# Optimization experiments

Hardware: AMD Instinct MI355X
Metric: run time of the kernel (lower is better)

## Reference

```python
import jax, jax.numpy as jnp
import numpy as np

B, L, D_MODEL, D_FF, H = 2, 2048, 512, 512, 8
DK = D_FF // H


def _lin(key, fan_in, fan_out):
    k1, k2 = jax.random.split(key)
    lim = 1.0 / np.sqrt(fan_in)
    W = jax.random.uniform(k1, (fan_in, fan_out), jnp.float32, -lim, lim)
    b = jax.random.uniform(k2, (fan_out,), jnp.float32, -lim, lim)
    return W, b


def setup_inputs() -> dict:
    key = jax.random.key(0)
    ks = jax.random.split(key, 13)
    x = jax.random.normal(ks[0], (B, L, D_MODEL), jnp.float32)
    x_knowledge = jax.random.normal(ks[1], (B, L, D_MODEL), jnp.float32)
    Wv, bv = _lin(ks[2], D_MODEL, D_FF)
    Wk, bk = _lin(ks[3], D_MODEL, D_FF)
    Wq, bq = _lin(ks[4], D_MODEL, D_FF)
    Wkf, bkf = _lin(ks[5], D_MODEL, D_FF)
    Wqf, bqf = _lin(ks[6], D_MODEL, D_FF)
    Wq2, bq2 = _lin(ks[7], D_FF, D_FF)
    Wk2, bk2 = _lin(ks[8], D_FF, D_FF)
    Wkf2, bkf2 = _lin(ks[9], D_FF, D_FF)
    Wqf2, bqf2 = _lin(ks[10], D_FF, D_FF)
    Wo, bo = _lin(ks[11], D_FF, D_MODEL)
    return dict(x=x, x_knowledge=x_knowledge, Wv=Wv, bv=bv, Wk=Wk, bk=bk,
                Wq=Wq, bq=bq, Wkf=Wkf, bkf=bkf, Wqf=Wqf, bqf=bqf,
                Wq2=Wq2, bq2=bq2, Wk2=Wk2, bk2=bk2, Wqf2=Wqf2, bqf2=bqf2,
                Wkf2=Wkf2, bkf2=bkf2, Wo=Wo, bo=bo)


def reference(x, x_knowledge, Wv, bv, Wk, bk, Wq, bq, Wkf, bkf, Wqf, bqf,
              Wq2, bq2, Wk2, bk2, Wqf2, bqf2, Wkf2, bkf2, Wo, bo):
    b, l, _ = x.shape
    # first projections from d_model -> d_ff
    v = x @ Wv + bv
    k = x @ Wk + bk
    q = x @ Wq + bq
    k_fei = x_knowledge @ Wkf + bkf
    q_fei = x_knowledge @ Wqf + bqf
    # second projections + NONSTANDARD head split: raw reshape (B,L,d_ff)->(B,h,L,dk)
    q = (q @ Wq2 + bq2).reshape(b, H, l, DK)
    k = (k @ Wk2 + bk2).reshape(b, H, l, DK)
    q_fei = (q_fei @ Wqf2 + bqf2).reshape(b, H, l, DK)
    k_fei = (k_fei @ Wkf2 + bkf2).reshape(b, H, l, DK)
    scale = 1.0 / np.sqrt(2.0 * DK).astype(np.float32)
    att = jnp.einsum('bhld,bhmd->bhlm', q, k) * scale
    att_fei = jnp.einsum('bhld,bhmd->bhlm', q_fei, k_fei) * scale
    score = jax.nn.softmax(att + att_fei, axis=-1)  # dropout is identity at eval
    v = v.reshape(b, H, l, DK)
    out = jnp.einsum('bhlm,bhmd->bhld', score, v).reshape(b, l, D_FF)
    return out @ Wo + bo
```

## Files before the change

kernel.cpp:

```cpp
#include <hip/hip_runtime.h>
#include <hip/hip_bf16.h>

typedef unsigned short u16;
typedef unsigned int   u32;
typedef __attribute__((ext_vector_type(8))) short bf16x8;
typedef __attribute__((ext_vector_type(4))) float f32x4;

#define SCALE 0.08838834764831845f
#define SCLOG 0.12752040542575836f

__device__ inline u16 f2bf(float f) {
  u32 u = __builtin_bit_cast(u32, f);
  u = (u + 0x7FFFu + ((u >> 16) & 1u)) >> 16;
  return (u16)u;
}
__device__ inline float bf2f(u16 b) {
  u32 u = (u32)b << 16;
  return __builtin_bit_cast(float, u);
}
__device__ inline u32 pkbf(float a, float b) {
  return (u32)f2bf(a) | ((u32)f2bf(b) << 16);
}

__device__ __forceinline__ void glds16(const u16* g, u16* l) {
  __builtin_amdgcn_global_load_lds(
      (__attribute__((address_space(1))) void*)g,
      (__attribute__((address_space(3))) void*)l, 16, 0, 0);
}

__global__ __launch_bounds__(256) void cvt_bf16(const float* __restrict__ a,
                                                const float* __restrict__ b,
                                                u16* __restrict__ oa,
                                                u16* __restrict__ ob) {
  const float* in = blockIdx.y ? b : a;
  u16* out = blockIdx.y ? ob : oa;
  const int i = (blockIdx.x * 256 + threadIdx.x) * 8;
  float4 f0 = *(const float4*)(in + i);
  float4 f1 = *(const float4*)(in + i + 4);
  alignas(16) u16 t[8] = {f2bf(f0.x), f2bf(f0.y), f2bf(f0.z), f2bf(f0.w),
                          f2bf(f1.x), f2bf(f1.y), f2bf(f1.z), f2bf(f1.w)};
  *(uint4*)(out + i) = *(const uint4*)t;
}

struct TPtrs { const float* p[10]; };

__global__ __launch_bounds__(256) void transposeW(TPtrs ptrs, u16* __restrict__ out) {
  __shared__ u16 ts[64][65];
  const float sc = (blockIdx.z == 5 || blockIdx.z == 7) ? SCLOG : 1.0f;
  const float* in = ptrs.p[blockIdx.z];
  u16* o = out + (size_t)blockIdx.z * 262144;
  const int t = threadIdx.x;
  const int k0 = blockIdx.y * 64, n0 = blockIdx.x * 64;
  for (int pp = 0; pp < 16; ++pp) {
    int id = t + 256 * pp; int r = id >> 6, c = id & 63;
    ts[r][c] = f2bf(in[(size_t)(k0 + r) * 512 + n0 + c] * sc);
  }
  __syncthreads();
  for (int pp = 0; pp < 16; ++pp) {
    int id = t + 256 * pp; int r = id >> 6, c = id & 63;
    o[(size_t)(n0 + r) * 512 + k0 + c] = ts[c][r];
  }
}

struct BPtrs { const float* p[10]; };

__global__ __launch_bounds__(512) void biasPack(BPtrs bp, float* __restrict__ out) {
  const int z = blockIdx.x, n = threadIdx.x;
  const float sc = (z == 5 || z == 7) ? SCLOG : 1.0f;
  out[z * 512 + n] = bp.p[z][n] * sc;
}

__global__ __launch_bounds__(256) void transposeV(const u16* __restrict__ v1,
                                                  u16* __restrict__ vt) {
  __shared__ u16 ts[64][65];
  const size_t base = (size_t)blockIdx.y * 131072;
  const u16* in = v1 + base;
  u16* out = vt + base;
  const int l0 = blockIdx.x * 64;
  const int t = threadIdx.x;
  const int r = t >> 3, c8 = (t & 7) * 8;
  for (int pp = 0; pp < 2; ++pp) {
    int rr = r + pp * 32;
    *(uint4*)&ts[rr][c8] = *(const uint4*)&in[(size_t)(l0 + rr) * 64 + c8];
  }
  __syncthreads();
  for (int pp = 0; pp < 2; ++pp) {
    int d = r + pp * 32;
    alignas(16) u16 tmp[8];
    #pragma unroll
    for (int i = 0; i < 8; ++i) tmp[i] = ts[c8 + i][d];
    *(uint4*)&out[(size_t)d * 2048 + l0 + c8] = *(const uint4*)tmp;
  }
}

struct GemmBatch {
  const u16* A[4];
  const u16* Ax;
  int xsplit;
  void* out[5];
  int wrow0, zstride;
};

template <typename TOUT>
__global__ __launch_bounds__(256, 4) void gemm4(GemmBatch gb,
    const u16* __restrict__ Wt, const float* __restrict__ biasP) {
  const int tx = blockIdx.x, z = blockIdx.z;
  const u16* A = (tx < gb.xsplit) ? gb.A[z] : gb.Ax;
  const int wrow = gb.wrow0 + z * gb.zstride + tx * 128;
  const int m0 = blockIdx.y * 128;
  const u16* B = Wt + (size_t)wrow * 512;
  const float* bias = biasP + wrow;

  const int t = threadIdx.x, wid = t >> 6, lane = t & 63;
  const int lg = lane >> 4, ln = lane & 15;
  const int wr = wid >> 1, wc = wid & 1;

  __shared__ u16 As[128][64];
  __shared__ u16 Bs[128][64];

  const u16* Ag = A + (size_t)m0 * 512;
  const int lrow = lane >> 3, lch = lane & 7;

  f32x4 acc[4][4];
  #pragma unroll
  for (int i = 0; i < 4; ++i)
    #pragma unroll
    for (int j = 0; j < 4; ++j)
      #pragma unroll
      for (int r = 0; r < 4; ++r) acc[i][j][r] = 0.0f;

  for (int kt = 0; kt < 8; ++kt) {
    #pragma unroll
    for (int c = 0; c < 4; ++c) {
      const int row = (wid * 4 + c) * 8 + lrow;
      const size_t go = (size_t)row * 512 + kt * 64 + lch * 8;
      glds16(Ag + go, &As[(wid * 4 + c) * 8][0]);
      glds16(B  + go, &Bs[(wid * 4 + c) * 8][0]);
    }
    __syncthreads();

    #pragma unroll
    for (int ck = 0; ck < 2; ++ck) {
      bf16x8 af[4], bfr[4];
      #pragma unroll
      for (int mi = 0; mi < 4; ++mi)
        af[mi] = *(const bf16x8*)&As[wr * 64 + mi * 16 + ln][ck * 32 + lg * 8];
      #pragma unroll
      for (int ni = 0; ni < 4; ++ni)
        bfr[ni] = *(const bf16x8*)&Bs[wc * 64 + ni * 16 + ln][ck * 32 + lg * 8];
      #pragma unroll
      for (int mi = 0; mi < 4; ++mi)
        #pragma unroll
        for (int ni = 0; ni < 4; ++ni)
          acc[mi][ni] = __builtin_amdgcn_mfma_f32_16x16x32_bf16(
              af[mi], bfr[ni], acc[mi][ni], 0, 0, 0);
    }
    if (kt < 7) __syncthreads();
  }

  TOUT* C = (TOUT*)gb.out[(wrow >> 9) - (gb.wrow0 >> 9)];
  const int nbase = wrow & 511;
  #pragma unroll
  for (int ni = 0; ni < 4; ++ni) {
    const int colw = wc * 64 + ni * 16 + ln;
    const float bv = bias[colw];
    const int col = nbase + colw;
    #pragma unroll
    for (int mi = 0; mi < 4; ++mi)
      #pragma unroll
      for (int r = 0; r < 4; ++r) {
        const int row = m0 + wr * 64 + mi * 16 + 4 * lg + r;
        const float val = acc[mi][ni][r] + bv;
        if constexpr (sizeof(TOUT) == 4) C[(size_t)row * 512 + col] = val;
        else                             C[(size_t)row * 512 + col] = f2bf(val);
      }
  }
}

__global__ __launch_bounds__(512) void attn7(
    const u16* __restrict__ q2, const u16* __restrict__ k2,
    const u16* __restrict__ qf2, const u16* __restrict__ kf2,
    const u16* __restrict__ vtg, u16* __restrict__ opart,
    float2* __restrict__ mlbuf) {
  const int id = blockIdx.x;
  const int nid = (id & 7) * 32 + (id >> 3);
  const int split = nid & 1;
  const int qt = (nid >> 1) & 7;
  const int bh = nid >> 4;
  const size_t base = (size_t)bh * 131072;
  const int kv0 = split * 1024;

  const u16* Q  = q2  + base;
  const u16* Qf = qf2 + base;
  u16* Op = opart + (size_t)split * 2097152 + base;

  const int t = threadIdx.x, wid = t >> 6, lane = t & 63;
  const int lg = lane >> 4, ln = lane & 15;
  const int r0 = qt * 256 + wid * 32;

  __shared__ u16 K_s [2][64][64];
  __shared__ u16 Kf_s[2][64][64];
  __shared__ u16 Vt_s[2][64][64];

  const int srow = t >> 3, sch = t & 7;
  const int fsr = (srow & 3) | (((srow >> 3) & 1) << 2);
  const int sw = (sch ^ fsr) * 8;
  const u16* Ksrc  = k2  + base + (size_t)(kv0 + srow) * 64 + sch * 8;
  const u16* Kfsrc = kf2 + base + (size_t)(kv0 + srow) * 64 + sch * 8;
  const u16* Vsrc  = vtg + base + (size_t)srow * 2048 + kv0 + sch * 8;

  bf16x8 aq[2][4];
  #pragma unroll
  for (int qb = 0; qb < 2; ++qb) {
    const int row = r0 + qb * 16 + ln;
    aq[qb][0] = *(const bf16x8*)&Q [row * 64 +      lg * 8];
    aq[qb][1] = *(const bf16x8*)&Q [row * 64 + 32 + lg * 8];
    aq[qb][2] = *(const bf16x8*)&Qf[row * 64 +      lg * 8];
    aq[qb][3] = *(const bf16x8*)&Qf[row * 64 + 32 + lg * 8];
  }

  f32x4 oacc[2][4];
  #pragma unroll
  for (int qb = 0; qb < 2; ++qb)
    #pragma unroll
    for (int df = 0; df < 4; ++df)
      #pragma unroll
      for (int r = 0; r < 4; ++r) oacc[qb][df][r] = 0.0f;
  float m_run[2], l_par[2];
  #pragma unroll
  for (int qb = 0; qb < 2; ++qb) { m_run[qb] = -1e30f; l_par[qb] = 0.0f; }

  const int rbase = 8 * (ln >> 2) + (ln & 3);

  uint4 rk = *(const uint4*)(Ksrc);
  uint4 rf = *(const uint4*)(Kfsrc);
  uint4 rv = *(const uint4*)(Vsrc);
  *(uint4*)&K_s [0][srow][sw] = rk;
  *(uint4*)&Kf_s[0][srow][sw] = rf;
  *(uint4*)&Vt_s[0][srow][sw] = rv;
  __syncthreads();

  int cur = 0;
  for (int kt = 0; kt < 16; ++kt) {
    if (kt < 15) {
      const int ko = (kt + 1) * 4096;
      rk = *(const uint4*)(Ksrc  + ko);
      rf = *(const uint4*)(Kfsrc + ko);
      rv = *(const uint4*)(Vsrc  + (kt + 1) * 64);
    }

    f32x4 s[2][4];
    #pragma unroll
    for (int m = 0; m < 4; ++m) {
      const int rowg = rbase + 4 * (m & 1) + 32 * (m >> 1);
      const int fz = (rowg & 3) | (((rowg >> 3) & 1) << 2);
      bf16x8 a0 = *(const bf16x8*)&K_s [cur][rowg][((0 + lg) ^ fz) * 8];
      bf16x8 a1 = *(const bf16x8*)&K_s [cur][rowg][((4 + lg) ^ fz) * 8];
      bf16x8 a2 = *(const bf16x8*)&Kf_s[cur][rowg][((0 + lg) ^ fz) * 8];
      bf16x8 a3 = *(const bf16x8*)&Kf_s[cur][rowg][((4 + lg) ^ fz) * 8];
      #pragma unroll
      for (int qb = 0; qb < 2; ++qb) {
        f32x4 a;
        #pragma unroll
        for (int r = 0; r < 4; ++r) a[r] = 0.0f;
        a = __builtin_amdgcn_mfma_f32_16x16x32_bf16(a0, aq[qb][0], a, 0, 0, 0);
        a = __builtin_amdgcn_mfma_f32_16x16x32_bf16(a1, aq[qb][1], a, 0, 0, 0);
        a = __builtin_amdgcn_mfma_f32_16x16x32_bf16(a2, aq[qb][2], a, 0, 0, 0);
        a = __builtin_amdgcn_mfma_f32_16x16x32_bf16(a3, aq[qb][3], a, 0, 0, 0);
        s[qb][m] = a;
      }
    }

    float smax[2];
    bool viol = false;
    #pragma unroll
    for (int qb = 0; qb < 2; ++qb) {
      float v = fmaxf(fmaxf(s[qb][0][0], s[qb][0][1]),
                      fmaxf(s[qb][0][2], s[qb][0][3]));
      #pragma unroll
      for (int m = 1; m < 4; ++m)
        v = fmaxf(v, fmaxf(fmaxf(s[qb][m][0], s[qb][m][1]),
                           fmaxf(s[qb][m][2], s[qb][m][3])));
      smax[qb] = v;
      viol = viol || (v > m_run[qb] + 11.0f);
    }
    if (__any(viol)) {
      float corrq[2];
      #pragma unroll
      for (int qb = 0; qb < 2; ++qb) {
        float v = smax[qb];
        v = fmaxf(v, __shfl_xor(v, 16, 64));
        v = fmaxf(v, __shfl_xor(v, 32, 64));
        const float mnew = fmaxf(m_run[qb], v);
        corrq[qb] = exp2f(m_run[qb] - mnew);
        m_run[qb] = mnew;
        l_par[qb] *= corrq[qb];
      }
      #pragma unroll
      for (int qb = 0; qb < 2; ++qb)
        #pragma unroll
        for (int r = 0; r < 4; ++r) {
          const float c = __shfl(corrq[qb], 4 * lg + r, 64);
          #pragma unroll
          for (int df = 0; df < 4; ++df) oacc[qb][df][r] *= c;
        }
    }

    bf16x8 pa[2][2];
    #pragma unroll
    for (int qb = 0; qb < 2; ++qb) {
      float pf[4][4];
      #pragma unroll
      for (int m = 0; m < 4; ++m)
        #pragma unroll
        for (int r = 0; r < 4; ++r) {
          const float p = exp2f(s[qb][m][r] - m_run[qb]);
          l_par[qb] += p;
          pf[m][r] = p;
        }
      #pragma unroll
      for (int kc = 0; kc < 2; ++kc) {
        union { u32 w[4]; bf16x8 v; } U;
        U.w[0] = pkbf(pf[2 * kc][0],     pf[2 * kc][1]);
        U.w[1] = pkbf(pf[2 * kc][2],     pf[2 * kc][3]);
        U.w[2] = pkbf(pf[2 * kc + 1][0], pf[2 * kc + 1][1]);
        U.w[3] = pkbf(pf[2 * kc + 1][2], pf[2 * kc + 1][3]);
        pa[qb][kc] = U.v;
      }
    }

    #pragma unroll
    for (int kc = 0; kc < 2; ++kc)
      #pragma unroll
      for (int df = 0; df < 4; ++df) {
        const int rv = 16 * df + ln;
        const int fz = (rv & 3) | (((rv >> 3) & 1) << 2);
        bf16x8 bv = *(const bf16x8*)&Vt_s[cur][rv][((kc * 4 + lg) ^ fz) * 8];
        oacc[0][df] = __builtin_amdgcn_mfma_f32_16x16x32_bf16(pa[0][kc], bv, oacc[0][df], 0, 0, 0);
        oacc[1][df] = __builtin_amdgcn_mfma_f32_16x16x32_bf16(pa[1][kc], bv, oacc[1][df], 0, 0, 0);
      }

    if (kt < 15) {
      *(uint4*)&K_s [cur ^ 1][srow][sw] = rk;
      *(uint4*)&Kf_s[cur ^ 1][srow][sw] = rf;
      *(uint4*)&Vt_s[cur ^ 1][srow][sw] = rv;
      __syncthreads();
      cur ^= 1;
    }
  }

  #pragma unroll
  for (int qb = 0; qb < 2; ++qb) {
    l_par[qb] += __shfl_xor(l_par[qb], 16, 64);
    l_par[qb] += __shfl_xor(l_par[qb], 32, 64);
  }

  #pragma unroll
  for (int qb = 0; qb < 2; ++qb)
    #pragma unroll
    for (int df = 0; df < 4; ++df)
      #pragma unroll
      for (int r = 0; r < 4; ++r) {
        const int row = r0 + qb * 16 + 4 * lg + r;
        const int col = df * 16 + ln;
        Op[(size_t)row * 64 + col] = f2bf(oacc[qb][df][r]);
      }
  if (lane < 16) {
    #pragma unroll
    for (int qb = 0; qb < 2; ++qb) {
      const int grow = bh * 2048 + r0 + qb * 16 + ln;
      mlbuf[split * 32768 + grow] = make_float2(m_run[qb], l_par[qb]);
    }
  }
}

__global__ __launch_bounds__(256) void combine(
    const u16* __restrict__ opart, const float2* __restrict__ mlbuf,
    u16* __restrict__ att) {
  const int gid = blockIdx.x * 256 + threadIdx.x;
  const int row = gid >> 3, c8 = (gid & 7) * 8;
  const float2 ml1 = mlbuf[row];
  const float2 ml2 = mlbuf[32768 + row];
  const float mx = fmaxf(ml1.x, ml2.x);
  const float a1 = exp2f(ml1.x - mx), a2 = exp2f(ml2.x - mx);
  const float inv = 1.0f / (ml1.y * a1 + ml2.y * a2);
  const float w1 = a1 * inv, w2 = a2 * inv;
  uint4 o1 = *(const uint4*)&opart[(size_t)row * 64 + c8];
  uint4 o2 = *(const uint4*)&opart[2097152 + (size_t)row * 64 + c8];
  const u16* p1 = (const u16*)&o1;
  const u16* p2 = (const u16*)&o2;
  alignas(16) u16 ot[8];
  #pragma unroll
  for (int i = 0; i < 8; ++i)
    ot[i] = f2bf(bf2f(p1[i]) * w1 + bf2f(p2[i]) * w2);
  *(uint4*)&att[(size_t)row * 64 + c8] = *(const uint4*)ot;
}

extern "C" void kernel_launch(void* const* d_in, const int* in_sizes, int n_in,
                              void* d_out, int out_size, void* d_ws, size_t ws_size,
                              hipStream_t stream) {
  const float* x    = (const float*)d_in[0];
  const float* xk   = (const float*)d_in[1];
  const float* Wv   = (const float*)d_in[2];  const float* bv   = (const float*)d_in[3];
  const float* Wk   = (const float*)d_in[4];  const float* bk   = (const float*)d_in[5];
  const float* Wq   = (const float*)d_in[6];  const float* bq   = (const float*)d_in[7];
  const float* Wkf  = (const float*)d_in[8];  const float* bkf  = (const float*)d_in[9];
  const float* Wqf  = (const float*)d_in[10]; const float* bqf  = (const float*)d_in[11];
  const float* Wq2  = (const float*)d_in[12]; const float* bq2  = (const float*)d_in[13];
  const float* Wk2  = (const float*)d_in[14]; const float* bk2  = (const float*)d_in[15];
  const float* Wqf2 = (const float*)d_in[16]; const float* bqf2 = (const float*)d_in[17];
  const float* Wkf2 = (const float*)d_in[18]; const float* bkf2 = (const float*)d_in[19];
  const float* Wo   = (const float*)d_in[20]; const float* bo   = (const float*)d_in[21];

  u16* ws = (u16*)d_ws;
  u16* Wt = ws;
  float* biasP = (float*)(ws + 2621440);
  u16* bufs = ws + 2621440 + 10240;
  const size_t BUF = 2097152;
  u16* v1  = bufs + 0 * BUF;
  u16* k1  = bufs + 1 * BUF;
  u16* q1  = bufs + 2 * BUF;
  u16* kf1 = bufs + 3 * BUF;
  u16* qf1 = bufs + 4 * BUF;
  u16* q2  = bufs + 5 * BUF;
  u16* k2  = bufs + 6 * BUF;
  u16* qf2 = bufs + 7 * BUF;
  u16* kf2 = bufs + 8 * BUF;
  float2* mlbuf = (float2*)(bufs + 9 * BUF);

  cvt_bf16<<<dim3(1024, 2), 256, 0, stream>>>(x, xk, q2, k2);

  TPtrs tp;
  tp.p[0] = Wv;  tp.p[1] = Wk;  tp.p[2] = Wq;   tp.p[3] = Wkf;  tp.p[4] = Wqf;
  tp.p[5] = Wq2; tp.p[6] = Wk2; tp.p[7] = Wqf2; tp.p[8] = Wkf2; tp.p[9] = Wo;
  transposeW<<<dim3(8, 8, 10), 256, 0, stream>>>(tp, Wt);

  BPtrs bp;
  bp.p[0] = bv;  bp.p[1] = bk;  bp.p[2] = bq;   bp.p[3] = bkf;  bp.p[4] = bqf;
  bp.p[5] = bq2; bp.p[6] = bk2; bp.p[7] = bqf2; bp.p[8] = bkf2; bp.p[9] = bo;
  biasPack<<<dim3(10), 512, 0, stream>>>(bp, biasP);

  GemmBatch g1 = {};
  g1.A[0] = q2;  g1.Ax = k2;  g1.xsplit = 12;
  g1.out[0] = v1; g1.out[1] = k1; g1.out[2] = q1; g1.out[3] = kf1; g1.out[4] = qf1;
  g1.wrow0 = 0; g1.zstride = 0;
  gemm4<u16><<<dim3(20, 32, 1), 256, 0, stream>>>(g1, Wt, biasP);

  GemmBatch g3 = {};
  g3.A[0] = q1; g3.A[1] = k1; g3.A[2] = qf1; g3.A[3] = kf1;
  g3.Ax = q1; g3.xsplit = 100;
  g3.out[0] = q2; g3.out[1] = k2; g3.out[2] = qf2; g3.out[3] = kf2;
  g3.wrow0 = 2560; g3.zstride = 512;
  gemm4<u16><<<dim3(4, 32, 4), 256, 0, stream>>>(g3, Wt, biasP);

  transposeV<<<dim3(32, 16), 256, 0, stream>>>(v1, q1);

  attn7<<<dim3(256), 512, 0, stream>>>(q2, k2, qf2, kf2, q1, kf1, mlbuf);

  combine<<<dim3(1024), 256, 0, stream>>>(kf1, mlbuf, v1);

  GemmBatch g4 = {};
  g4.A[0] = v1; g4.Ax = v1; g4.xsplit = 100;
  g4.out[0] = d_out;
  g4.wrow0 = 4608; g4.zstride = 0;
  gemm4<float><<<dim3(4, 32, 1), 256, 0, stream>>>(g4, Wt, biasP);
}
```

Baseline: 117.9 us.

## Fuse split-KV combine into output GEMM and bias pack into weight transpose

Removes the separate combine kernel by merging the two split-KV partial outputs, rescaled by their max and sum statistics, directly in the output projection GEMM's A-tile load. It also folds the bias packing into the weight transpose kernel and uses the hardware exp2 and bf16 conversion intrinsics in attention. This saves two launches and a round trip of the attention output through global memory. The cost is that the output GEMM now does a synchronous register load plus combine arithmetic instead of the async global-to-LDS copy, and repeats the combine work across its four column tiles.

```diff
diff --git a/kernel.cpp b/kernel.cpp
--- a/kernel.cpp
+++ b/kernel.cpp
@@ -18,8 +18,18 @@
   u32 u = (u32)b << 16;
   return __builtin_bit_cast(float, u);
 }
-__device__ inline u32 pkbf(float a, float b) {
-  return (u32)f2bf(a) | ((u32)f2bf(b) << 16);
+__device__ __forceinline__ u16 cvbf(float f) {
+  return __builtin_bit_cast(u16, __float2bfloat16(f));
+}
+__device__ __forceinline__ u32 pkbf(float a, float b) {
+  return (u32)cvbf(a) | ((u32)cvbf(b) << 16);
+}
+__device__ __forceinline__ float fexp2(float x) {
+#if __has_builtin(__builtin_amdgcn_exp2f)
+  return __builtin_amdgcn_exp2f(x);
+#else
+  float r; asm("v_exp_f32 %0, %1" : "=v"(r) : "v"(x)); return r;
+#endif
 }
 
 __device__ __forceinline__ void glds16(const u16* g, u16* l) {
@@ -42,15 +52,21 @@
   *(uint4*)(out + i) = *(const uint4*)t;
 }
 
-struct TPtrs { const float* p[10]; };
-
-__global__ __launch_bounds__(256) void transposeW(TPtrs ptrs, u16* __restrict__ out) {
+struct WPtrs { const float* w[10]; const float* b[10]; };
+
+__global__ __launch_bounds__(256) void transposeW(WPtrs p, u16* __restrict__ out,
+                                                  float* __restrict__ biasP) {
   __shared__ u16 ts[64][65];
-  const float sc = (blockIdx.z == 5 || blockIdx.z == 7) ? SCLOG : 1.0f;
-  const float* in = ptrs.p[blockIdx.z];
-  u16* o = out + (size_t)blockIdx.z * 262144;
+  const int z = blockIdx.z;
+  const float sc = (z == 5 || z == 7) ? SCLOG : 1.0f;
+  const float* in = p.w[z];
+  u16* o = out + (size_t)z * 262144;
   const int t = threadIdx.x;
   const int k0 = blockIdx.y * 64, n0 = blockIdx.x * 64;
+  if (blockIdx.x == 0 && blockIdx.y == 0) {
+    biasP[z * 512 + t]       = p.b[z][t] * sc;
+    biasP[z * 512 + t + 256] = p.b[z][t + 256] * sc;
+  }
   for (int pp = 0; pp < 16; ++pp) {
     int id = t + 256 * pp; int r = id >> 6, c = id & 63;
     ts[r][c] = f2bf(in[(size_t)(k0 + r) * 512 + n0 + c] * sc);
@@ -60,14 +76,6 @@
     int id = t + 256 * pp; int r = id >> 6, c = id & 63;
     o[(size_t)(n0 + r) * 512 + k0 + c] = ts[c][r];
   }
-}
-
-struct BPtrs { const float* p[10]; };
-
-__global__ __launch_bounds__(512) void biasPack(BPtrs bp, float* __restrict__ out) {
-  const int z = blockIdx.x, n = threadIdx.x;
-  const float sc = (z == 5 || z == 7) ? SCLOG : 1.0f;
-  out[z * 512 + n] = bp.p[z][n] * sc;
 }
 
 __global__ __launch_bounds__(256) void transposeV(const u16* __restrict__ v1,
@@ -99,9 +107,10 @@
   int xsplit;
   void* out[5];
   int wrow0, zstride;
+  const float2* ml;
 };
 
-template <typename TOUT>
+template <typename TOUT, bool FC>
 __global__ __launch_bounds__(256, 4) void gemm4(GemmBatch gb,
     const u16* __restrict__ Wt, const float* __restrict__ biasP) {
   const int tx = blockIdx.x, z = blockIdx.z;
@@ -133,9 +142,30 @@
     #pragma unroll
     for (int c = 0; c < 4; ++c) {
       const int row = (wid * 4 + c) * 8 + lrow;
-      const size_t go = (size_t)row * 512 + kt * 64 + lch * 8;
-      glds16(Ag + go, &As[(wid * 4 + c) * 8][0]);
-      glds16(B  + go, &Bs[(wid * 4 + c) * 8][0]);
+      if constexpr (FC) {
+        const int rc = (m0 + row) * 8 + kt;
+        const float2 ml1 = gb.ml[rc];
+        const float2 ml2 = gb.ml[32768 + rc];
+        const float mx = fmaxf(ml1.x, ml2.x);
+        const float a1 = fexp2(ml1.x - mx), a2 = fexp2(ml2.x - mx);
+        const float inv = 1.0f / (ml1.y * a1 + ml2.y * a2);
+        const float w1 = a1 * inv, w2 = a2 * inv;
+        const size_t off = (size_t)rc * 64 + lch * 8;
+        uint4 o1 = *(const uint4*)(A + off);
+        uint4 o2 = *(const uint4*)(A + 2097152 + off);
+        const u16* p1 = (const u16*)&o1;
+        const u16* p2 = (const u16*)&o2;
+        alignas(16) u16 tmp[8];
+        #pragma unroll
+        for (int i = 0; i < 8; ++i)
+          tmp[i] = cvbf(bf2f(p1[i]) * w1 + bf2f(p2[i]) * w2);
+        *(uint4*)&As[(wid * 4 + c) * 8 + lrow][lch * 8] = *(const uint4*)tmp;
+      } else {
+        glds16(Ag + (size_t)row * 512 + kt * 64 + lch * 8,
+               &As[(wid * 4 + c) * 8][0]);
+      }
+      glds16(B + (size_t)row * 512 + kt * 64 + lch * 8,
+             &Bs[(wid * 4 + c) * 8][0]);
     }
     __syncthreads();
 
@@ -177,7 +207,7 @@
   }
 }
 
-__global__ __launch_bounds__(512) void attn7(
+__global__ __launch_bounds__(512) void attn8(
     const u16* __restrict__ q2, const u16* __restrict__ k2,
     const u16* __restrict__ qf2, const u16* __restrict__ kf2,
     const u16* __restrict__ vtg, u16* __restrict__ opart,
@@ -292,7 +322,7 @@
         v = fmaxf(v, __shfl_xor(v, 16, 64));
         v = fmaxf(v, __shfl_xor(v, 32, 64));
         const float mnew = fmaxf(m_run[qb], v);
-        corrq[qb] = exp2f(m_run[qb] - mnew);
+        corrq[qb] = fexp2(m_run[qb] - mnew);
         m_run[qb] = mnew;
         l_par[qb] *= corrq[qb];
       }
@@ -314,7 +344,7 @@
       for (int m = 0; m < 4; ++m)
         #pragma unroll
         for (int r = 0; r < 4; ++r) {
-          const float p = exp2f(s[qb][m][r] - m_run[qb]);
+          const float p = fexp2(s[qb][m][r] - m_run[qb]);
           l_par[qb] += p;
           pf[m][r] = p;
         }
@@ -372,28 +402,6 @@
       mlbuf[split * 32768 + grow] = make_float2(m_run[qb], l_par[qb]);
     }
   }
-}
-
-__global__ __launch_bounds__(256) void combine(
-    const u16* __restrict__ opart, const float2* __restrict__ mlbuf,
-    u16* __restrict__ att) {
-  const int gid = blockIdx.x * 256 + threadIdx.x;
-  const int row = gid >> 3, c8 = (gid & 7) * 8;
-  const float2 ml1 = mlbuf[row];
-  const float2 ml2 = mlbuf[32768 + row];
-  const float mx = fmaxf(ml1.x, ml2.x);
-  const float a1 = exp2f(ml1.x - mx), a2 = exp2f(ml2.x - mx);
-  const float inv = 1.0f / (ml1.y * a1 + ml2.y * a2);
-  const float w1 = a1 * inv, w2 = a2 * inv;
-  uint4 o1 = *(const uint4*)&opart[(size_t)row * 64 + c8];
-  uint4 o2 = *(const uint4*)&opart[2097152 + (size_t)row * 64 + c8];
-  const u16* p1 = (const u16*)&o1;
-  const u16* p2 = (const u16*)&o2;
-  alignas(16) u16 ot[8];
-  #pragma unroll
-  for (int i = 0; i < 8; ++i)
-    ot[i] = f2bf(bf2f(p1[i]) * w1 + bf2f(p2[i]) * w2);
-  *(uint4*)&att[(size_t)row * 64 + c8] = *(const uint4*)ot;
 }
 
 extern "C" void kernel_launch(void* const* d_in, const int* in_sizes, int n_in,
@@ -430,38 +438,34 @@
 
   cvt_bf16<<<dim3(1024, 2), 256, 0, stream>>>(x, xk, q2, k2);
 
-  TPtrs tp;
-  tp.p[0] = Wv;  tp.p[1] = Wk;  tp.p[2] = Wq;   tp.p[3] = Wkf;  tp.p[4] = Wqf;
-  tp.p[5] = Wq2; tp.p[6] = Wk2; tp.p[7] = Wqf2; tp.p[8] = Wkf2; tp.p[9] = Wo;
-  transposeW<<<dim3(8, 8, 10), 256, 0, stream>>>(tp, Wt);
-
-  BPtrs bp;
-  bp.p[0] = bv;  bp.p[1] = bk;  bp.p[2] = bq;   bp.p[3] = bkf;  bp.p[4] = bqf;
-  bp.p[5] = bq2; bp.p[6] = bk2; bp.p[7] = bqf2; bp.p[8] = bkf2; bp.p[9] = bo;
-  biasPack<<<dim3(10), 512, 0, stream>>>(bp, biasP);
+  WPtrs wp;
+  wp.w[0] = Wv;  wp.w[1] = Wk;  wp.w[2] = Wq;   wp.w[3] = Wkf;  wp.w[4] = Wqf;
+  wp.w[5] = Wq2; wp.w[6] = Wk2; wp.w[7] = Wqf2; wp.w[8] = Wkf2; wp.w[9] = Wo;
+  wp.b[0] = bv;  wp.b[1] = bk;  wp.b[2] = bq;   wp.b[3] = bkf;  wp.b[4] = bqf;
+  wp.b[5] = bq2; wp.b[6] = bk2; wp.b[7] = bqf2; wp.b[8] = bkf2; wp.b[9] = bo;
+  transposeW<<<dim3(8, 8, 10), 256, 0, stream>>>(wp, Wt, biasP);
 
   GemmBatch g1 = {};
   g1.A[0] = q2;  g1.Ax = k2;  g1.xsplit = 12;
   g1.out[0] = v1; g1.out[1] = k1; g1.out[2] = q1; g1.out[3] = kf1; g1.out[4] = qf1;
   g1.wrow0 = 0; g1.zstride = 0;
-  gemm4<u16><<<dim3(20, 32, 1), 256, 0, stream>>>(g1, Wt, biasP);
+  gemm4<u16, false><<<dim3(20, 32, 1), 256, 0, stream>>>(g1, Wt, biasP);
 
   GemmBatch g3 = {};
   g3.A[0] = q1; g3.A[1] = k1; g3.A[2] = qf1; g3.A[3] = kf1;
   g3.Ax = q1; g3.xsplit = 100;
   g3.out[0] = q2; g3.out[1] = k2; g3.out[2] = qf2; g3.out[3] = kf2;
   g3.wrow0 = 2560; g3.zstride = 512;
-  gemm4<u16><<<dim3(4, 32, 4), 256, 0, stream>>>(g3, Wt, biasP);
+  gemm4<u16, false><<<dim3(4, 32, 4), 256, 0, stream>>>(g3, Wt, biasP);
 
   transposeV<<<dim3(32, 16), 256, 0, stream>>>(v1, q1);
 
-  attn7<<<dim3(256), 512, 0, stream>>>(q2, k2, qf2, kf2, q1, kf1, mlbuf);
-
-  combine<<<dim3(1024), 256, 0, stream>>>(kf1, mlbuf, v1);
+  attn8<<<dim3(256), 512, 0, stream>>>(q2, k2, qf2, kf2, q1, kf1, mlbuf);
 
   GemmBatch g4 = {};
-  g4.A[0] = v1; g4.Ax = v1; g4.xsplit = 100;
+  g4.A[0] = kf1; g4.Ax = kf1; g4.xsplit = 100;
   g4.out[0] = d_out;
   g4.wrow0 = 4608; g4.zstride = 0;
-  gemm4<float><<<dim3(4, 32, 1), 256, 0, stream>>>(g4, Wt, biasP);
-}
+  g4.ml = (const float2*)mlbuf;
+  gemm4<float, true><<<dim3(4, 32, 1), 256, 0, stream>>>(g4, Wt, biasP);
+}
```

Measured after the change: 127.1 us. 7.8% more time.
